# Performance work log

Hardware: AMD Instinct MI355X
Metric: run time of the kernel (lower is better)

Reference implementation:

```python
import jax, jax.numpy as jnp
import numpy as np

D = 256  # rst_input_dim


def _gru_cell(x, h, W_ih, W_hh, b_ih, b_hh):
    # x, h: (..., D); W_*: (3D, D); PyTorch GRU gate order: r, z, n
    gi = x @ W_ih.T + b_ih          # (..., 3D)
    gh = h @ W_hh.T + b_hh
    i_r, i_z, i_n = jnp.split(gi, 3, axis=-1)
    h_r, h_z, h_n = jnp.split(gh, 3, axis=-1)
    r = jax.nn.sigmoid(i_r + h_r)
    z = jax.nn.sigmoid(i_z + h_z)
    n = jnp.tanh(i_n + r * h_n)
    return (1.0 - z) * n + z * h


def setup_inputs() -> dict:
    key = jax.random.key(0)
    ks = jax.random.split(key, 5)
    B, L = 32, 4096
    s = 1.0 / np.sqrt(D)
    return {
        "leaf_embeds": jax.random.normal(ks[0], (B, L, D), dtype=jnp.float32),
        "W_ih": jax.random.normal(ks[1], (3 * D, D), dtype=jnp.float32) * s,
        "W_hh": jax.random.normal(ks[2], (3 * D, D), dtype=jnp.float32) * s,
        "b_ih": jax.random.normal(ks[3], (3 * D,), dtype=jnp.float32) * s,
        "b_hh": jax.random.normal(ks[4], (3 * D,), dtype=jnp.float32) * s,
    }


def reference(leaf_embeds, W_ih, W_hh, b_ih, b_hh):
    # Post-order traversal of a perfect binary tree, batched level-by-level
    # (classic tree-RNN same-depth batching). Leaves: embed = EDU embedding,
    # hidden = zeros. Internal node: h0 = mean(h_left, h_right); run GRU over
    # the 2-step sequence [left_embed, right_embed]; out = mean of the two
    # GRU outputs; returned hidden = final GRU hidden.
    embeds = leaf_embeds                      # (B, N, D)
    hs = jnp.zeros_like(leaf_embeds)          # (B, N, D)
    n = embeds.shape[1]
    while n > 1:
        xL, xR = embeds[:, 0::2], embeds[:, 1::2]   # (B, n/2, D)
        hL, hR = hs[:, 0::2], hs[:, 1::2]
        h0 = 0.5 * (hL + hR)                         # mean of child hiddens
        h1 = _gru_cell(xL, h0, W_ih, W_hh, b_ih, b_hh)
        h2 = _gru_cell(xR, h1, W_ih, W_hh, b_ih, b_hh)
        embeds = 0.5 * (h1 + h2)                     # mean over seq outputs
        hs = h2
        n //= 2
    return embeds[:, 0]                              # (B, D): root embedding
```

## Files before the change

### kernel.cpp

```cpp
#include <hip/hip_runtime.h>
#include <hip/hip_bf16.h>
#include <stdint.h>

typedef _Float16 f16x8 __attribute__((ext_vector_type(8)));
typedef float    f32x4 __attribute__((ext_vector_type(4)));

#define GLDS16(gptr, lptr) \
  __builtin_amdgcn_global_load_lds((const __attribute__((address_space(1))) void*)(gptr), \
                                   (__attribute__((address_space(3))) void*)(lptr), 16, 0, 0)

__global__ __launch_bounds__(256) void prepack_weights(
    const float* __restrict__ Wih, const float* __restrict__ Whh,
    const float* __restrict__ bih, const float* __restrict__ bhh,
    _Float16* __restrict__ WP, float* __restrict__ BC)
{
    if (blockIdx.x == 2048) {
        int i = threadIdx.x;
        BC[i]       = bih[i] + bhh[i];
        BC[256 + i] = bih[256 + i] + bhh[256 + i];
        BC[512 + i] = bih[512 + i];
        BC[768 + i] = bhh[512 + i];
        return;
    }
    int idx = blockIdx.x * 256 + threadIdx.x;
    int j   = idx & 7;
    int nl  = (idx >> 3) & 63;
    int sub = (idx >> 9) & 7;
    int g   = (idx >> 12) & 3;
    int d0b = (idx >> 14) & 3;
    int c   = idx >> 16;
    int k = c * 64 + sub * 8 + j;
    int d = d0b * 64 + nl;
    float v = 0.f;
    if (g == 0)      v = (k < 256) ? Wih[d * 256 + k]         : Whh[d * 256 + (k - 256)];
    else if (g == 1) v = (k < 256) ? Wih[(256 + d) * 256 + k] : Whh[(256 + d) * 256 + (k - 256)];
    else if (g == 2) v = (k < 256) ? Wih[(512 + d) * 256 + k] : 0.f;
    else             v = (k >= 256) ? Whh[(512 + d) * 256 + (k - 256)] : 0.f;
    WP[idx] = (_Float16)v;
}

__global__ __launch_bounds__(256) void convert_split(
    const float* __restrict__ leaf, _Float16* __restrict__ XE, _Float16* __restrict__ XO)
{
    int t = blockIdx.x * 256 + threadIdx.x;
    size_t e = (size_t)t * 4;
    int row = (int)(e >> 8), col = (int)(e & 255);
    float4 v = *(const float4*)(leaf + e);
    _Float16* dst = ((row & 1) ? XO : XE) + ((size_t)(row >> 1) * 256 + col);
    union { _Float16 h[4]; uint64_t u; } p;
    p.h[0] = (_Float16)v.x; p.h[1] = (_Float16)v.y;
    p.h[2] = (_Float16)v.z; p.h[3] = (_Float16)v.w;
    *(uint64_t*)dst = p.u;
}

template<int MT, bool SWIZ>
__global__ __launch_bounds__(256, (MT == 8) ? 2 : 3) void gru_cell(
    const _Float16* __restrict__ Xsrc,
    const _Float16* __restrict__ Hsrc,
    const _Float16* __restrict__ WP,
    const float* __restrict__ BC,
    _Float16* __restrict__ Hout,
    _Float16* __restrict__ Ee, _Float16* __restrict__ Eo, _Float16* __restrict__ HP,
    int M)
{
    constexpr int AROW = MT * 16 * 8 + 8;
    constexpr int ASZ  = 8 * AROW;
    constexpr int BROW = 520;
    __shared__ __align__(16) _Float16 Alds[2 * ASZ];
    __shared__ __align__(16) _Float16 Blds[3 * 8 * BROW];

    const int tid  = threadIdx.x;
    int bm, d0b;
    if (SWIZ) {
        int xcd = blockIdx.x & 7, slot = blockIdx.x >> 3;
        d0b = slot & 3;
        bm  = (slot >> 2) * 8 + xcd;
    } else {
        bm = blockIdx.x >> 2; d0b = blockIdx.x & 3;
    }
    const int m0   = bm * (MT * 16);
    const int wave = tid >> 6, lane = tid & 63;
    const int quad = lane >> 4, lo = lane & 15;

    const bool has_h = (Hsrc != nullptr);
    const int nch = has_h ? 8 : 4;

    f32x4 acc[MT][4];
#pragma unroll
    for (int a = 0; a < MT; ++a)
#pragma unroll
        for (int b = 0; b < 4; ++b) acc[a][b] = (f32x4){0.f, 0.f, 0.f, 0.f};
    float hinv[MT][4];

    auto issueA = [&](int c) {
        const _Float16* base = (c < 4) ? Xsrc : Hsrc;
        const int coloff = (c & 3) * 64;
        _Float16* Ab = Alds + (c & 1) * ASZ;
        constexpr int IPS = MT / 4;
#pragma unroll
        for (int i = 0; i < MT / 2; ++i) {
            int ai = wave * (MT / 2) + i;
            int sub = ai / IPS, mh = ai % IPS;
            int row = m0 + mh * 64 + lane;
            if (MT == 4 && row >= M) row = M - 1;
            GLDS16(base + (size_t)row * 256 + coloff + sub * 8,
                   Ab + sub * AROW + mh * 64 * 8);
        }
    };

    issueA(0);

    for (int c = 0; c < nch; ++c) {
        __syncthreads();
        {
            const size_t cb = (size_t)(c * 4 + d0b) * 4;
#pragma unroll
            for (int i = 0; i < 6; ++i) {
                int bi = wave * 6 + i;
                int slot = bi >> 3, sub = bi & 7;
                int g = (slot == 2) ? ((c < 4) ? 2 : 3) : slot;
                GLDS16(WP + ((cb + g) * 8 + sub) * 512 + lane * 8,
                       Blds + (slot * 8 + sub) * BROW);
            }
        }
        __syncthreads();
        if (c + 1 < nch) issueA(c + 1);

        const _Float16* Ab = Alds + (c & 1) * ASZ;
#pragma unroll
        for (int ks = 0; ks < 2; ++ks) {
            const int subb = ks * 4 + quad;
            f16x8 af[MT];
#pragma unroll
            for (int mt = 0; mt < MT; ++mt)
                af[mt] = *(const f16x8*)(Ab + subb * AROW + (mt * 16 + lo) * 8);
            f16x8 b0 = *(const f16x8*)(Blds + (0 * 8 + subb) * BROW + (wave * 16 + lo) * 8);
            f16x8 b1 = *(const f16x8*)(Blds + (1 * 8 + subb) * BROW + (wave * 16 + lo) * 8);
            f16x8 b2 = *(const f16x8*)(Blds + (2 * 8 + subb) * BROW + (wave * 16 + lo) * 8);
#pragma unroll
            for (int mt = 0; mt < MT; ++mt)
                acc[mt][0] = __builtin_amdgcn_mfma_f32_16x16x32_f16(af[mt], b0, acc[mt][0], 0, 0, 0);
#pragma unroll
            for (int mt = 0; mt < MT; ++mt)
                acc[mt][1] = __builtin_amdgcn_mfma_f32_16x16x32_f16(af[mt], b1, acc[mt][1], 0, 0, 0);
            if (c < 4) {
#pragma unroll
                for (int mt = 0; mt < MT; ++mt)
                    acc[mt][2] = __builtin_amdgcn_mfma_f32_16x16x32_f16(af[mt], b2, acc[mt][2], 0, 0, 0);
            } else {
#pragma unroll
                for (int mt = 0; mt < MT; ++mt)
                    acc[mt][3] = __builtin_amdgcn_mfma_f32_16x16x32_f16(af[mt], b2, acc[mt][3], 0, 0, 0);
            }
        }

        if (has_h && c == 4 + d0b) {
            const int colw = wave * 16 + lo;
            const int sub = colw >> 3, j = colw & 7;
#pragma unroll
            for (int mt = 0; mt < MT; ++mt)
#pragma unroll
                for (int r = 0; r < 4; ++r)
                    hinv[mt][r] = (float)Ab[sub * AROW + (mt * 16 + quad * 4 + r) * 8 + j];
        }
    }

    const int d = d0b * 64 + wave * 16 + lo;
    const float brz0 = BC[d];
    const float brz1 = BC[256 + d];
    const float bni  = BC[512 + d];
    const float bnh  = BC[768 + d];
#pragma unroll
    for (int mt = 0; mt < MT; ++mt) {
        const int mbase = m0 + mt * 16 + quad * 4;
        float hq[4], h1v[4];
#pragma unroll
        for (int r = 0; r < 4; ++r) {
            float hin = has_h ? hinv[mt][r] : 0.f;
            h1v[r] = hin;
            float rg = 1.f / (1.f + __expf(-(acc[mt][0][r] + brz0)));
            float zg = 1.f / (1.f + __expf(-(acc[mt][1][r] + brz1)));
            float ex = __expf(2.f * (acc[mt][2][r] + bni + rg * (acc[mt][3][r] + bnh)));
            float nv = 1.f - 2.f / (ex + 1.f);
            hq[r] = (1.f - zg) * nv + zg * hin;
        }
        if (Hout) {
#pragma unroll
            for (int r = 0; r < 4; ++r)
                if (MT == 8 || mbase + r < M)
                    Hout[(size_t)(mbase + r) * 256 + d] = (_Float16)hq[r];
        } else {
#pragma unroll
            for (int r = 0; r < 4; ++r) {
                int m = mbase + r;
                if (MT == 8 || m < M)
                    (((m & 1) ? Eo : Ee))[(size_t)(m >> 1) * 256 + d] =
                        (_Float16)(0.5f * (h1v[r] + hq[r]));
            }
            if (MT == 8 || mbase + 1 < M)
                HP[(size_t)(mbase >> 1) * 256 + d] = (_Float16)(0.5f * (hq[0] + hq[1]));
            if (MT == 8 || mbase + 3 < M)
                HP[(size_t)((mbase >> 1) + 1) * 256 + d] = (_Float16)(0.5f * (hq[2] + hq[3]));
        }
    }
}

__global__ __launch_bounds__(256) void final_out(
    const _Float16* __restrict__ XE, const _Float16* __restrict__ XO,
    float* __restrict__ out)
{
    int i = blockIdx.x * 256 + threadIdx.x;
    int j = i >> 8, col = i & 255;
    const _Float16* src = (j & 1) ? XO : XE;
    out[i] = (float)src[(size_t)(j >> 1) * 256 + col];
}

extern "C" void kernel_launch(void* const* d_in, const int* in_sizes, int n_in,
                              void* d_out, int out_size, void* d_ws, size_t ws_size,
                              hipStream_t stream) {
    const float* leaf = (const float*)d_in[0];
    const float* Wih  = (const float*)d_in[1];
    const float* Whh  = (const float*)d_in[2];
    const float* bih  = (const float*)d_in[3];
    const float* bhh  = (const float*)d_in[4];

    char* ws = (char*)d_ws;
    _Float16* WPp = (_Float16*)ws;
    _Float16* XAe = (_Float16*)(ws + (1ull  << 20));
    _Float16* XAo = (_Float16*)(ws + (33ull << 20));
    _Float16* XBe = (_Float16*)(ws + (65ull << 20));
    _Float16* XBo = (_Float16*)(ws + (81ull << 20));
    _Float16* H1  = (_Float16*)(ws + (97ull << 20));
    _Float16* HPb = (_Float16*)(ws + (129ull << 20));
    float*    BCp = (float*)(ws + (145ull << 20));

    prepack_weights<<<2049, 256, 0, stream>>>(Wih, Whh, bih, bhh, WPp, BCp);
    convert_split<<<32768, 256, 0, stream>>>(leaf, XAe, XAo);

    _Float16 *XeC = XAe, *XoC = XAo, *XeN = XBe, *XoN = XBo;
    const _Float16* hp = nullptr;
    int M = 65536;
    for (int lev = 0; lev < 12; ++lev) {
        if (M >= 8192) {
            int grid = (M / 128) * 4;
            gru_cell<8, true><<<grid, 256, 0, stream>>>(XeC, hp, WPp, BCp,
                                                        H1, nullptr, nullptr, nullptr, M);
            gru_cell<8, true><<<grid, 256, 0, stream>>>(XoC, H1, WPp, BCp,
                                                        nullptr, XeN, XoN, HPb, M);
        } else {
            int nbm = (M + 63) / 64;
            int grid = nbm * 4;
            if ((nbm & 7) == 0) {
                gru_cell<4, true><<<grid, 256, 0, stream>>>(XeC, hp, WPp, BCp,
                                                            H1, nullptr, nullptr, nullptr, M);
                gru_cell<4, true><<<grid, 256, 0, stream>>>(XoC, H1, WPp, BCp,
                                                            nullptr, XeN, XoN, HPb, M);
            } else {
                gru_cell<4, false><<<grid, 256, 0, stream>>>(XeC, hp, WPp, BCp,
                                                             H1, nullptr, nullptr, nullptr, M);
                gru_cell<4, false><<<grid, 256, 0, stream>>>(XoC, H1, WPp, BCp,
                                                             nullptr, XeN, XoN, HPb, M);
            }
        }
        hp = HPb;
        _Float16* t;
        t = XeC; XeC = XeN; XeN = t;
        t = XoC; XoC = XoN; XoN = t;
        M >>= 1;
    }
    final_out<<<32, 256, 0, stream>>>(XeC, XoC, (float*)d_out);
}
```

Baseline: 730.5 us.

## Load activations directly from global into registers and double-buffer weights in LDS

Removes the LDS staging of the activation (A) tiles. Each lane now reads its f16x8 fragments straight from global memory, and the freed LDS holds double-buffered weight (B) tiles, which drops one __syncthreads per chunk. The hidden input for the epilogue is re-read from global instead of being captured from LDS. This cuts LDS traffic and barriers, but exposes global-load latency inside the MFMA loop, uses strided uncoalesced row reads, and raises the launch bound to 3 blocks for MT=8, which may force register spills.

```diff
diff --git a/kernel.cpp b/kernel.cpp
--- a/kernel.cpp
+++ b/kernel.cpp
@@ -54,7 +54,7 @@
 }
 
 template<int MT, bool SWIZ>
-__global__ __launch_bounds__(256, (MT == 8) ? 2 : 3) void gru_cell(
+__global__ __launch_bounds__(256, 3) void gru_cell(
     const _Float16* __restrict__ Xsrc,
     const _Float16* __restrict__ Hsrc,
     const _Float16* __restrict__ WP,
@@ -63,11 +63,9 @@
     _Float16* __restrict__ Ee, _Float16* __restrict__ Eo, _Float16* __restrict__ HP,
     int M)
 {
-    constexpr int AROW = MT * 16 * 8 + 8;
-    constexpr int ASZ  = 8 * AROW;
     constexpr int BROW = 520;
-    __shared__ __align__(16) _Float16 Alds[2 * ASZ];
-    __shared__ __align__(16) _Float16 Blds[3 * 8 * BROW];
+    constexpr int BSZ  = 3 * 8 * BROW;
+    __shared__ __align__(16) _Float16 Blds[2 * BSZ];
 
     const int tid  = threadIdx.x;
     int bm, d0b;
@@ -79,7 +77,8 @@
         bm = blockIdx.x >> 2; d0b = blockIdx.x & 3;
     }
     const int m0   = bm * (MT * 16);
-    const int wave = tid >> 6, lane = tid & 63;
+    const int tidw = tid;
+    const int wave = tidw >> 6, lane = tidw & 63;
     const int quad = lane >> 4, lo = lane & 15;
 
     const bool has_h = (Hsrc != nullptr);
@@ -90,78 +89,57 @@
     for (int a = 0; a < MT; ++a)
 #pragma unroll
         for (int b = 0; b < 4; ++b) acc[a][b] = (f32x4){0.f, 0.f, 0.f, 0.f};
-    float hinv[MT][4];
-
-    auto issueA = [&](int c) {
-        const _Float16* base = (c < 4) ? Xsrc : Hsrc;
-        const int coloff = (c & 3) * 64;
-        _Float16* Ab = Alds + (c & 1) * ASZ;
-        constexpr int IPS = MT / 4;
-#pragma unroll
-        for (int i = 0; i < MT / 2; ++i) {
-            int ai = wave * (MT / 2) + i;
-            int sub = ai / IPS, mh = ai % IPS;
-            int row = m0 + mh * 64 + lane;
-            if (MT == 4 && row >= M) row = M - 1;
-            GLDS16(base + (size_t)row * 256 + coloff + sub * 8,
-                   Ab + sub * AROW + mh * 64 * 8);
+
+    auto issueB = [&](int c) {
+        const size_t cb = (size_t)(c * 4 + d0b) * 4;
+        _Float16* dstb = Blds + (c & 1) * BSZ;
+#pragma unroll
+        for (int i = 0; i < 6; ++i) {
+            int bi = wave * 6 + i;
+            int slot = bi >> 3, sub = bi & 7;
+            int g = (slot == 2) ? ((c < 4) ? 2 : 3) : slot;
+            GLDS16(WP + ((cb + g) * 8 + sub) * 512 + lane * 8,
+                   dstb + (slot * 8 + sub) * BROW);
         }
     };
 
-    issueA(0);
+    issueB(0);
 
     for (int c = 0; c < nch; ++c) {
         __syncthreads();
-        {
-            const size_t cb = (size_t)(c * 4 + d0b) * 4;
-#pragma unroll
-            for (int i = 0; i < 6; ++i) {
-                int bi = wave * 6 + i;
-                int slot = bi >> 3, sub = bi & 7;
-                int g = (slot == 2) ? ((c < 4) ? 2 : 3) : slot;
-                GLDS16(WP + ((cb + g) * 8 + sub) * 512 + lane * 8,
-                       Blds + (slot * 8 + sub) * BROW);
-            }
-        }
-        __syncthreads();
-        if (c + 1 < nch) issueA(c + 1);
-
-        const _Float16* Ab = Alds + (c & 1) * ASZ;
+        if (c + 1 < nch) issueB(c + 1);
+
+        const _Float16* Bb = Blds + (c & 1) * BSZ;
+        const _Float16* abase = ((c < 4) ? Xsrc : Hsrc) + (size_t)(c & 3) * 64 + quad * 8;
 #pragma unroll
         for (int ks = 0; ks < 2; ++ks) {
             const int subb = ks * 4 + quad;
-            f16x8 af[MT];
-#pragma unroll
-            for (int mt = 0; mt < MT; ++mt)
-                af[mt] = *(const f16x8*)(Ab + subb * AROW + (mt * 16 + lo) * 8);
-            f16x8 b0 = *(const f16x8*)(Blds + (0 * 8 + subb) * BROW + (wave * 16 + lo) * 8);
-            f16x8 b1 = *(const f16x8*)(Blds + (1 * 8 + subb) * BROW + (wave * 16 + lo) * 8);
-            f16x8 b2 = *(const f16x8*)(Blds + (2 * 8 + subb) * BROW + (wave * 16 + lo) * 8);
-#pragma unroll
-            for (int mt = 0; mt < MT; ++mt)
-                acc[mt][0] = __builtin_amdgcn_mfma_f32_16x16x32_f16(af[mt], b0, acc[mt][0], 0, 0, 0);
-#pragma unroll
-            for (int mt = 0; mt < MT; ++mt)
-                acc[mt][1] = __builtin_amdgcn_mfma_f32_16x16x32_f16(af[mt], b1, acc[mt][1], 0, 0, 0);
+            const _Float16* brow = Bb + subb * BROW + (wave * 16 + lo) * 8;
+            f16x8 b0 = *(const f16x8*)(brow);
+            f16x8 b1 = *(const f16x8*)(brow + 8 * BROW);
+            f16x8 b2 = *(const f16x8*)(brow + 16 * BROW);
+            const _Float16* ak = abase + ks * 32;
             if (c < 4) {
 #pragma unroll
-                for (int mt = 0; mt < MT; ++mt)
-                    acc[mt][2] = __builtin_amdgcn_mfma_f32_16x16x32_f16(af[mt], b2, acc[mt][2], 0, 0, 0);
+                for (int mt = 0; mt < MT; ++mt) {
+                    int row = m0 + mt * 16 + lo;
+                    if (MT == 4 && row >= M) row = M - 1;
+                    f16x8 af = *(const f16x8*)(ak + (size_t)row * 256);
+                    acc[mt][0] = __builtin_amdgcn_mfma_f32_16x16x32_f16(af, b0, acc[mt][0], 0, 0, 0);
+                    acc[mt][1] = __builtin_amdgcn_mfma_f32_16x16x32_f16(af, b1, acc[mt][1], 0, 0, 0);
+                    acc[mt][2] = __builtin_amdgcn_mfma_f32_16x16x32_f16(af, b2, acc[mt][2], 0, 0, 0);
+                }
             } else {
 #pragma unroll
-                for (int mt = 0; mt < MT; ++mt)
-                    acc[mt][3] = __builtin_amdgcn_mfma_f32_16x16x32_f16(af[mt], b2, acc[mt][3], 0, 0, 0);
+                for (int mt = 0; mt < MT; ++mt) {
+                    int row = m0 + mt * 16 + lo;
+                    if (MT == 4 && row >= M) row = M - 1;
+                    f16x8 af = *(const f16x8*)(ak + (size_t)row * 256);
+                    acc[mt][0] = __builtin_amdgcn_mfma_f32_16x16x32_f16(af, b0, acc[mt][0], 0, 0, 0);
+                    acc[mt][1] = __builtin_amdgcn_mfma_f32_16x16x32_f16(af, b1, acc[mt][1], 0, 0, 0);
+                    acc[mt][3] = __builtin_amdgcn_mfma_f32_16x16x32_f16(af, b2, acc[mt][3], 0, 0, 0);
+                }
             }
-        }
-
-        if (has_h && c == 4 + d0b) {
-            const int colw = wave * 16 + lo;
-            const int sub = colw >> 3, j = colw & 7;
-#pragma unroll
-            for (int mt = 0; mt < MT; ++mt)
-#pragma unroll
-                for (int r = 0; r < 4; ++r)
-                    hinv[mt][r] = (float)Ab[sub * AROW + (mt * 16 + quad * 4 + r) * 8 + j];
         }
     }
 
@@ -176,7 +154,9 @@
         float hq[4], h1v[4];
 #pragma unroll
         for (int r = 0; r < 4; ++r) {
-            float hin = has_h ? hinv[mt][r] : 0.f;
+            int m = mbase + r;
+            int mm = (MT == 8) ? m : ((m < M) ? m : (M - 1));
+            float hin = has_h ? (float)Hsrc[(size_t)mm * 256 + d] : 0.f;
             h1v[r] = hin;
             float rg = 1.f / (1.f + __expf(-(acc[mt][0][r] + brz0)));
             float zg = 1.f / (1.f + __expf(-(acc[mt][1][r] + brz1)));
```

New measurement: 1.287 ms. 1.76x slower.
